# Optimization experiments

Hardware: AMD Instinct MI355X
Metric: run time of the kernel (lower is better)

Reference implementation:

```python
import jax, jax.numpy as jnp
import numpy as np

B, S, H, NH, NL, G, D, A, T = 32, 512, 512, 8, 6, 8, 256, 18, 1024
HD = H // NH


def setup_inputs() -> dict:
    key = jax.random.key(0)
    ks = jax.random.split(key, 32)
    def n(k, shape, s=0.02):
        return jax.random.normal(k, shape, jnp.float32) * s
    return {
        'game_indices': jax.random.randint(ks[0], (B,), 0, G),
        'states': jax.random.normal(ks[1], (B, S, D), jnp.float32),
        'actions': jax.random.randint(ks[2], (B, S), 0, A),
        'returns_to_go': jax.random.normal(ks[3], (B, S), jnp.float32),
        'timesteps': jax.random.randint(ks[4], (B, S), 0, T),
        'attention_mask': jnp.ones((B, S), jnp.int32),
        'game_emb': n(ks[5], (G, H)),
        'obs_W': n(ks[6], (G, D, H)),
        'obs_b': n(ks[7], (G, H)),
        'obs_ln_g': jnp.ones((G, H), jnp.float32),
        'obs_ln_b': jnp.zeros((G, H), jnp.float32),
        'act_emb': n(ks[8], (G, A, H)),
        'ret_W': n(ks[9], (H,)),
        'ret_b': n(ks[10], (H,)),
        'time_emb': n(ks[11], (T, H)),
        'Wqkv': n(ks[12], (NL, 3 * H, H)),
        'bqkv': n(ks[13], (NL, 3 * H)),
        'Wo': n(ks[14], (NL, H, H)),
        'bo': n(ks[15], (NL, H)),
        'ln1_g': jnp.ones((NL, H), jnp.float32),
        'ln1_b': jnp.zeros((NL, H), jnp.float32),
        'W1': n(ks[16], (NL, 4 * H, H)),
        'b1': n(ks[17], (NL, 4 * H)),
        'W2': n(ks[18], (NL, H, 4 * H)),
        'b2': n(ks[19], (NL, H)),
        'ln2_g': jnp.ones((NL, H), jnp.float32),
        'ln2_b': jnp.zeros((NL, H), jnp.float32),
        'sh_W': n(ks[20], (G, H, D)),
        'sh_b': n(ks[21], (G, D)),
        'ah_W': n(ks[22], (G, H, A)),
        'ah_b': n(ks[23], (G, A)),
        'rh_W': n(ks[24], (H, 1)),
        'rh_b': n(ks[25], (1,)),
    }


def _ln(x, g, b, eps=1e-5):
    m = jnp.mean(x, -1, keepdims=True)
    v = jnp.mean((x - m) ** 2, -1, keepdims=True)
    return (x - m) / jnp.sqrt(v + eps) * g + b


def reference(game_indices, states, actions, returns_to_go, timesteps, attention_mask,
              game_emb, obs_W, obs_b, obs_ln_g, obs_ln_b, act_emb, ret_W, ret_b, time_emb,
              Wqkv, bqkv, Wo, bo, ln1_g, ln1_b, W1, b1, W2, b2, ln2_g, ln2_b,
              sh_W, sh_b, ah_W, ah_b, rh_W, rh_b):
    gi = game_indices
    g_emb = game_emb[gi][:, None, :]  # [B,1,H]
    # per-game routed observation embedding: Linear -> LayerNorm -> ReLU (grouped GEMM by game)
    se = jnp.einsum('bsd,bdh->bsh', states, obs_W[gi]) + obs_b[gi][:, None, :]
    se = jax.nn.relu(_ln(se, obs_ln_g[gi][:, None, :], obs_ln_b[gi][:, None, :]))
    # per-game routed action embedding table lookup
    ae = act_emb[gi[:, None], actions]  # [B,S,H]
    re = returns_to_go[..., None] * ret_W + ret_b  # Linear(1,H)
    te = time_emb[timesteps]
    x = se + ae + re + te + g_emb
    # key padding mask (src_key_padding_mask: True where attention_mask==0)
    bias = jnp.where((attention_mask == 0)[:, None, None, :], -1e9, 0.0)  # [B,1,1,S]
    scale = 1.0 / jnp.sqrt(jnp.asarray(HD, jnp.float32))
    for l in range(NL):  # post-norm TransformerEncoderLayer, relu, dropout=0 (eval)
        qkv = jnp.einsum('bsh,oh->bso', x, Wqkv[l]) + bqkv[l]
        q, k, v = jnp.split(qkv, 3, axis=-1)
        q = q.reshape(B, S, NH, HD).transpose(0, 2, 1, 3)
        k = k.reshape(B, S, NH, HD).transpose(0, 2, 1, 3)
        v = v.reshape(B, S, NH, HD).transpose(0, 2, 1, 3)
        scores = jnp.einsum('bhqd,bhkd->bhqk', q, k) * scale + bias
        attn = jnp.einsum('bhqk,bhkd->bhqd', jax.nn.softmax(scores, -1), v)
        attn = attn.transpose(0, 2, 1, 3).reshape(B, S, H)
        attn = jnp.einsum('bsh,oh->bso', attn, Wo[l]) + bo[l]
        x = _ln(x + attn, ln1_g[l], ln1_b[l])
        ff = jax.nn.relu(jnp.einsum('bsh,fh->bsf', x, W1[l]) + b1[l])
        ff = jnp.einsum('bsf,hf->bsh', ff, W2[l]) + b2[l]
        x = _ln(x + ff, ln2_g[l], ln2_b[l])
    # per-game routed prediction heads
    state_preds = jnp.einsum('bsh,bho->bso', x, sh_W[gi]) + sh_b[gi][:, None, :]
    action_preds = jnp.einsum('bsh,bho->bso', x, ah_W[gi]) + ah_b[gi][:, None, :]
    return_preds = x @ rh_W + rh_b
    return (state_preds, action_preds, return_preds)
```

## Files before the change

kernel.cpp:

```cpp
#include <hip/hip_runtime.h>

typedef __bf16 bf16x4 __attribute__((ext_vector_type(4)));
typedef __bf16 bf16x8 __attribute__((ext_vector_type(8)));
typedef float f32x4 __attribute__((ext_vector_type(4)));
typedef int int4v __attribute__((ext_vector_type(4)));

#define C1SM  0.18033688011112042592f

typedef const __attribute__((address_space(1))) void gvoid_t;
typedef __attribute__((address_space(3))) void lvoid_t;


__global__ void cvt_f32_bf16(const float* __restrict__ src, __bf16* __restrict__ dst, int n4)
{
    int i = blockIdx.x * blockDim.x + threadIdx.x;
    if (i >= n4) return;
    f32x4 v = *reinterpret_cast<const f32x4*>(src + (size_t)i * 4);
    bf16x4 o;
    #pragma unroll
    for (int k = 0; k < 4; ++k) o[k] = (__bf16)v[k];
    *reinterpret_cast<bf16x4*>(dst + (size_t)i * 4) = o;
}

__global__ void transpose_cvt(const float* __restrict__ src, __bf16* __restrict__ dst, int R, int C)
{
    int m = blockIdx.y;
    int n = R * C;
    int i = blockIdx.x * 256 + threadIdx.x;
    if (i >= n) return;
    int c = i / R, r = i - c * R;
    dst[(size_t)m * n + i] = (__bf16)src[(size_t)m * n + (size_t)r * C + c];
}

__global__ void transpose_f32(const float* __restrict__ src, float* __restrict__ dst, int R, int C)
{
    int m = blockIdx.y;
    int n = R * C;
    int i = blockIdx.x * 256 + threadIdx.x;
    if (i >= n) return;
    int c = i / R, r = i - c * R;
    dst[(size_t)m * n + i] = src[(size_t)m * n + (size_t)r * C + c];
}

__global__ __launch_bounds__(256, 4)
void gemm_bt(const __bf16* __restrict__ A, size_t strideA,
             const __bf16* __restrict__ B, size_t strideB,
             const float* __restrict__ bias, int strideBias,
             float* Cf, __bf16* Cb, size_t strideC,
             const int* __restrict__ gidx,
             int K, int ldc, int relu, __bf16* __restrict__ vt)
{
    __shared__ __align__(16) char smem[32768];
    __bf16* lCb = (__bf16*)smem;
    float*  lCf = (float*)smem;

    const int z = blockIdx.z;
    const int g = gidx ? gidx[z] : 0;
    const __bf16* Ab = A + (size_t)z * strideA;
    const __bf16* Bb = B + (size_t)g * strideB;

    const int nx = gridDim.x;
    const int nwg = nx * gridDim.y;
    int orig = blockIdx.y * nx + blockIdx.x;
    int wg = ((nwg & 7) == 0) ? ((orig & 7) * (nwg >> 3) + (orig >> 3)) : orig;
    const int bm = (wg / nx) * 128, bn = (wg % nx) * 128;

    const int t = threadIdx.x;
    const int w = t >> 6, lane = t & 63;
    const int wr = (w >> 1) * 64, wc = (w & 1) * 64;
    const int l16 = lane & 15, lk = lane >> 4;

    const int srow = lane >> 2;
    const int schunk = (lane & 3) ^ (srow & 3);
    const int ca = (lk ^ (l16 & 3)) * 8;

    f32x4 acc[4][4] = {};

    auto stage = [&](int buf, int kt) {
        __bf16* la = (__bf16*)(smem + buf * 16384);
        __bf16* lb = la + 4096;
        #pragma unroll
        for (int jj = 0; jj < 2; ++jj) {
            const __bf16* ga = Ab + (size_t)(bm + w * 32 + jj * 16 + srow) * K + kt + schunk * 8;
            __builtin_amdgcn_global_load_lds((gvoid_t*)ga, (lvoid_t*)&la[(w * 32 + jj * 16) * 32], 16, 0, 0);
            const __bf16* gb = Bb + (size_t)(bn + w * 32 + jj * 16 + srow) * K + kt + schunk * 8;
            __builtin_amdgcn_global_load_lds((gvoid_t*)gb, (lvoid_t*)&lb[(w * 32 + jj * 16) * 32], 16, 0, 0);
        }
    };

    stage(0, 0);
    __syncthreads();
    int cur = 0;
    for (int kt = 0; kt < K; kt += 32) {
        if (kt + 32 < K) stage(cur ^ 1, kt + 32);
        __bf16* la = (__bf16*)(smem + cur * 16384);
        __bf16* lb = la + 4096;
        bf16x8 af[4], bfr[4];
        #pragma unroll
        for (int i = 0; i < 4; ++i) {
            af[i]  = *reinterpret_cast<const bf16x8*>(&la[(wr + i * 16 + l16) * 32 + ca]);
            bfr[i] = *reinterpret_cast<const bf16x8*>(&lb[(wc + i * 16 + l16) * 32 + ca]);
        }
        #pragma unroll
        for (int mi = 0; mi < 4; ++mi)
            #pragma unroll
            for (int ni = 0; ni < 4; ++ni)
                acc[mi][ni] = __builtin_amdgcn_mfma_f32_16x16x32_bf16(af[mi], bfr[ni], acc[mi][ni], 0, 0, 0);
        __syncthreads();
        cur ^= 1;
    }

    const float* biasb = bias ? bias + (size_t)g * strideBias : nullptr;

    if (vt && bn >= 1024) {
        const int bb = bm >> 9;
        const int s0 = (bm & 511) + wr + lk * 4;
        #pragma unroll
        for (int ni = 0; ni < 4; ++ni) {
            int c = bn + wc + ni * 16 + l16;
            float bv = biasb ? biasb[c] : 0.f;
            int hh = (c - 1024) >> 6, d = c & 63;
            __bf16* vrow = vt + ((size_t)(bb * 8 + hh) * 64 + d) * 512;
            #pragma unroll
            for (int mi = 0; mi < 4; ++mi) {
                bf16x4 o;
                #pragma unroll
                for (int j = 0; j < 4; ++j) o[j] = (__bf16)(acc[mi][ni][j] + bv);
                *reinterpret_cast<bf16x4*>(vrow + s0 + mi * 16) = o;
            }
        }
        return;
    }

    if (Cb) {
        #pragma unroll
        for (int ni = 0; ni < 4; ++ni) {
            int col = wc + ni * 16 + l16;
            float bv = biasb ? biasb[bn + col] : 0.f;
            #pragma unroll
            for (int mi = 0; mi < 4; ++mi)
                #pragma unroll
                for (int j = 0; j < 4; ++j) {
                    float v = acc[mi][ni][j] + bv;
                    if (relu) v = fmaxf(v, 0.f);
                    lCb[(wr + mi * 16 + lk * 4 + j) * 128 + col] = (__bf16)v;
                }
        }
        __syncthreads();
        #pragma unroll
        for (int it = 0; it < 8; ++it) {
            int off = it * 2048 + t * 8;
            int rl = off >> 7, col = off & 127;
            *reinterpret_cast<int4v*>(Cb + (size_t)z * strideC + (size_t)(bm + rl) * ldc + bn + col) =
                *reinterpret_cast<const int4v*>(&lCb[off]);
        }
    } else {
        #pragma unroll
        for (int p = 0; p < 2; ++p) {
            if (p) __syncthreads();
            if (wr == p * 64) {
                #pragma unroll
                for (int ni = 0; ni < 4; ++ni) {
                    int col = wc + ni * 16 + l16;
                    float bv = biasb ? biasb[bn + col] : 0.f;
                    #pragma unroll
                    for (int mi = 0; mi < 4; ++mi)
                        #pragma unroll
                        for (int j = 0; j < 4; ++j) {
                            float v = acc[mi][ni][j] + bv;
                            if (relu) v = fmaxf(v, 0.f);
                            lCf[(mi * 16 + lk * 4 + j) * 128 + col] = v;
                        }
                }
            }
            __syncthreads();
            #pragma unroll
            for (int it = 0; it < 8; ++it) {
                int off = it * 1024 + t * 4;
                int rl = off >> 7, col = off & 127;
                *reinterpret_cast<f32x4*>(Cf + (size_t)z * strideC + (size_t)(bm + p * 64 + rl) * ldc + bn + col) =
                    *reinterpret_cast<const f32x4*>(&lCf[off]);
            }
        }
    }
}

__global__ __launch_bounds__(256, 4)
void attn_fwd(const __bf16* __restrict__ qkv, const __bf16* __restrict__ vt,
              const int* __restrict__ mask, __bf16* __restrict__ out)
{
    __shared__ __bf16 lK[128 * 64];
    __shared__ __bf16 lP[4][16 * 32];
    __shared__ float lM2[128];

    const int bh = blockIdx.x;
    const int b = bh >> 3, h = bh & 7;
    const int q0 = blockIdx.y * 64;
    const int t = threadIdx.x, w = t >> 6, lane = t & 63;
    const int l16 = lane & 15, lk = lane >> 4;

    const __bf16* qbase = qkv + (size_t)b * 512 * 1536 + h * 64;
    const __bf16* kbase = qbase + 512;
    const __bf16* vtb = vt + (size_t)(b * 8 + h) * 64 * 512;

    bf16x8 qfr[2];
    {
        int row = q0 + w * 16 + l16;
        #pragma unroll
        for (int kc = 0; kc < 2; ++kc)
            qfr[kc] = *reinterpret_cast<const bf16x8*>(qbase + (size_t)row * 1536 + (kc * 4 + lk) * 8);
    }

    float m_run = -1e30f, l_run = 0.f;
    f32x4 oacc[4] = {};
    const int xsw = ((l16 >> 1) & 3) << 1;

    for (int kt = 0; kt < 512; kt += 128) {
        __syncthreads();
        #pragma unroll
        for (int r = 0; r < 4; ++r) {
            int c = t + r * 256;
            int row = c >> 3, ch = c & 7;
            *reinterpret_cast<int4v*>(&lK[row * 64 + ((ch ^ (row & 7)) * 8)]) =
                *reinterpret_cast<const int4v*>(kbase + (size_t)(kt + row) * 1536 + ch * 8);
        }
        if (t < 128) lM2[t] = (mask[b * 512 + kt + t] == 0) ? -2e9f : 0.f;
        __syncthreads();

        f32x4 sacc[8] = {};
        #pragma unroll
        for (int ni = 0; ni < 8; ++ni) {
            int krow = ni * 16 + l16;
            #pragma unroll
            for (int kc = 0; kc < 2; ++kc) {
                bf16x8 kf = *reinterpret_cast<const bf16x8*>(&lK[krow * 64 + (((kc * 4 + lk) ^ (krow & 7)) * 8)]);
                sacc[ni] = __builtin_amdgcn_mfma_f32_16x16x32_bf16(kf, qfr[kc], sacc[ni], 0, 0, 0);
            }
        }

        float mx = -3e38f;
        #pragma unroll
        for (int ni = 0; ni < 8; ++ni) {
            f32x4 mkv = *reinterpret_cast<const f32x4*>(&lM2[ni * 16 + lk * 4]);
            #pragma unroll
            for (int j = 0; j < 4; ++j) {
                float sv = fmaf(sacc[ni][j], C1SM, mkv[j]);
                sacc[ni][j] = sv;
                mx = fmaxf(mx, sv);
            }
        }
        mx = fmaxf(mx, __shfl_xor(mx, 16));
        mx = fmaxf(mx, __shfl_xor(mx, 32));
        bool need = mx > m_run + 11.54f;
        if (__any((int)need)) {
            float mn = fmaxf(m_run, mx);
            float alpha = exp2f(m_run - mn);
            m_run = mn;
            l_run *= alpha;
            #pragma unroll
            for (int j = 0; j < 4; ++j) {
                float aj = __shfl(alpha, lk * 4 + j);
                #pragma unroll
                for (int dn = 0; dn < 4; ++dn) oacc[dn][j] *= aj;
            }
        }
        float ps = 0.f;
        #pragma unroll
        for (int ni = 0; ni < 8; ++ni)
            #pragma unroll
            for (int j = 0; j < 4; ++j) {
                float p = exp2f(sacc[ni][j] - m_run);
                sacc[ni][j] = p;
                ps += p;
            }
        l_run += ps;

        __bf16* lp = &lP[w][0];
        #pragma unroll
        for (int kc = 0; kc < 4; ++kc) {
            #pragma unroll
            for (int n2 = 0; n2 < 2; ++n2) {
                bf16x4 o;
                #pragma unroll
                for (int j = 0; j < 4; ++j) o[j] = (__bf16)sacc[kc * 2 + n2][j];
                *reinterpret_cast<bf16x4*>(&lp[l16 * 32 + ((n2 * 4 + lk) ^ xsw) * 4]) = o;
            }
            bf16x8 pf = *reinterpret_cast<const bf16x8*>(&lp[l16 * 32 + (lk ^ (xsw >> 1)) * 8]);
            #pragma unroll
            for (int dn = 0; dn < 4; ++dn) {
                bf16x8 vf = *reinterpret_cast<const bf16x8*>(vtb + (size_t)(dn * 16 + l16) * 512 + kt + kc * 32 + lk * 8);
                oacc[dn] = __builtin_amdgcn_mfma_f32_16x16x32_bf16(pf, vf, oacc[dn], 0, 0, 0);
            }
        }
    }

    float s = l_run;
    s += __shfl_xor(s, 16);
    s += __shfl_xor(s, 32);
    float linv = 1.f / s;
    #pragma unroll
    for (int j = 0; j < 4; ++j) {
        float lj = __shfl(linv, lk * 4 + j);
        #pragma unroll
        for (int dn = 0; dn < 4; ++dn) {
            int row = q0 + w * 16 + lk * 4 + j;
            int col = h * 64 + dn * 16 + l16;
            out[(size_t)(b * 512 + row) * 512 + col] = (__bf16)(oacc[dn][j] * lj);
        }
    }
}


__device__ __forceinline__ float wsum64(float v)
{
    #pragma unroll
    for (int d = 32; d >= 1; d >>= 1) v += __shfl_xor(v, d);
    return v;
}

__global__ __launch_bounds__(256)
void ln_fuse(const float* resid, const __bf16* __restrict__ proj,
             const float* __restrict__ gamma, const float* __restrict__ beta,
             float* xfo, __bf16* __restrict__ xbo)
{
    int tok = blockIdx.x * 4 + (threadIdx.x >> 6);
    int lane = threadIdx.x & 63;
    size_t base = (size_t)tok * 512 + lane * 8;
    float y[8];
    {
        f32x4 a0 = *reinterpret_cast<const f32x4*>(resid + base);
        f32x4 a1 = *reinterpret_cast<const f32x4*>(resid + base + 4);
        bf16x8 pv = *reinterpret_cast<const bf16x8*>(proj + base);
        #pragma unroll
        for (int i = 0; i < 4; ++i) { y[i] = a0[i] + (float)pv[i]; y[4 + i] = a1[i] + (float)pv[4 + i]; }
    }
    float s = 0.f;
    #pragma unroll
    for (int i = 0; i < 8; ++i) s += y[i];
    float mean = wsum64(s) * (1.f / 512.f);
    float v = 0.f;
    #pragma unroll
    for (int i = 0; i < 8; ++i) { float d = y[i] - mean; v += d * d; }
    float rstd = rsqrtf(wsum64(v) * (1.f / 512.f) + 1e-5f);
    int hh = lane * 8;
    f32x4 g0 = *reinterpret_cast<const f32x4*>(gamma + hh);
    f32x4 g1 = *reinterpret_cast<const f32x4*>(gamma + hh + 4);
    f32x4 b0 = *reinterpret_cast<const f32x4*>(beta + hh);
    f32x4 b1 = *reinterpret_cast<const f32x4*>(beta + hh + 4);
    f32x4 o0, o1;
    bf16x8 ob;
    #pragma unroll
    for (int i = 0; i < 4; ++i) {
        float t0 = (y[i] - mean) * rstd * g0[i] + b0[i];
        float t1 = (y[4 + i] - mean) * rstd * g1[i] + b1[i];
        o0[i] = t0; o1[i] = t1;
        ob[i] = (__bf16)t0; ob[4 + i] = (__bf16)t1;
    }
    *reinterpret_cast<f32x4*>(xfo + base) = o0;
    *reinterpret_cast<f32x4*>(xfo + base + 4) = o1;
    *reinterpret_cast<bf16x8*>(xbo + base) = ob;
}

__global__ __launch_bounds__(256)
void embed_fin(const __bf16* __restrict__ seraw, const int* __restrict__ gi,
               const int* __restrict__ actions, const float* __restrict__ rtg,
               const int* __restrict__ ts,
               const float* __restrict__ olg, const float* __restrict__ olb,
               const float* __restrict__ act_emb, const float* __restrict__ retW,
               const float* __restrict__ retb, const float* __restrict__ time_emb,
               const float* __restrict__ game_emb,
               float* __restrict__ xfo, __bf16* __restrict__ xbo)
{
    int tok = blockIdx.x * 4 + (threadIdx.x >> 6);
    int lane = threadIdx.x & 63;
    int b = tok >> 9;
    int g = gi[b];
    int a = actions[tok];
    int tt = ts[tok];
    float rv = rtg[tok];
    size_t base = (size_t)tok * 512 + lane * 8;
    int hh = lane * 8;

    float y[8];
    {
        bf16x8 a0 = *reinterpret_cast<const bf16x8*>(seraw + base);
        #pragma unroll
        for (int i = 0; i < 8; ++i) y[i] = (float)a0[i];
    }
    float s = 0.f;
    #pragma unroll
    for (int i = 0; i < 8; ++i) s += y[i];
    float mean = wsum64(s) * (1.f / 512.f);
    float v = 0.f;
    #pragma unroll
    for (int i = 0; i < 8; ++i) { float d = y[i] - mean; v += d * d; }
    float rstd = rsqrtf(wsum64(v) * (1.f / 512.f) + 1e-5f);

    const float* gp = olg + (size_t)g * 512 + hh;
    const float* bp = olb + (size_t)g * 512 + hh;
    const float* ap = act_emb + ((size_t)g * 18 + a) * 512 + hh;
    const float* tp = time_emb + (size_t)tt * 512 + hh;
    const float* ep = game_emb + (size_t)g * 512 + hh;
    const float* rwp = retW + hh;
    const float* rbp = retb + hh;

    f32x4 o0, o1;
    bf16x8 ob;
    #pragma unroll
    for (int half = 0; half < 2; ++half) {
        f32x4 gv = *reinterpret_cast<const f32x4*>(gp + half * 4);
        f32x4 bv = *reinterpret_cast<const f32x4*>(bp + half * 4);
        f32x4 av = *reinterpret_cast<const f32x4*>(ap + half * 4);
        f32x4 tv = *reinterpret_cast<const f32x4*>(tp + half * 4);
        f32x4 ev = *reinterpret_cast<const f32x4*>(ep + half * 4);
        f32x4 rw = *reinterpret_cast<const f32x4*>(rwp + half * 4);
        f32x4 rb = *reinterpret_cast<const f32x4*>(rbp + half * 4);
        #pragma unroll
        for (int i = 0; i < 4; ++i) {
            float n = (y[half * 4 + i] - mean) * rstd * gv[i] + bv[i];
            n = fmaxf(n, 0.f);
            float o = n + av[i] + rv * rw[i] + rb[i] + tv[i] + ev[i];
            if (half == 0) o0[i] = o; else o1[i] = o;
            ob[half * 4 + i] = (__bf16)o;
        }
    }
    *reinterpret_cast<f32x4*>(xfo + base) = o0;
    *reinterpret_cast<f32x4*>(xfo + base + 4) = o1;
    *reinterpret_cast<bf16x8*>(xbo + base) = ob;
}

__global__ __launch_bounds__(256)
void head_ar(const float* __restrict__ xf, const int* __restrict__ gi,
             const float* __restrict__ ahWt, const float* __restrict__ ah_b,
             const float* __restrict__ rhW, const float* __restrict__ rhb,
             float* __restrict__ outA, float* __restrict__ outR)
{
    int tok = blockIdx.x * 4 + (threadIdx.x >> 6);
    int lane = threadIdx.x & 63;
    int b = tok >> 9;
    int g = gi[b];
    size_t base = (size_t)tok * 512 + lane * 8;
    float x[8];
    {
        f32x4 a0 = *reinterpret_cast<const f32x4*>(xf + base);
        f32x4 a1 = *reinterpret_cast<const f32x4*>(xf + base + 4);
        #pragma unroll
        for (int i = 0; i < 4; ++i) { x[i] = a0[i]; x[4 + i] = a1[i]; }
    }
    #pragma unroll 1
    for (int a = 0; a < 18; ++a) {
        const float* wp = ahWt + ((size_t)g * 18 + a) * 512 + lane * 8;
        f32x4 w0 = *reinterpret_cast<const f32x4*>(wp);
        f32x4 w1 = *reinterpret_cast<const f32x4*>(wp + 4);
        float p = 0.f;
        #pragma unroll
        for (int i = 0; i < 4; ++i) { p += x[i] * w0[i]; p += x[4 + i] * w1[i]; }
        p = wsum64(p);
        if (lane == 0) outA[(size_t)tok * 18 + a] = p + ah_b[g * 18 + a];
    }
    {
        const float* wp = rhW + lane * 8;
        f32x4 w0 = *reinterpret_cast<const f32x4*>(wp);
        f32x4 w1 = *reinterpret_cast<const f32x4*>(wp + 4);
        float p = 0.f;
        #pragma unroll
        for (int i = 0; i < 4; ++i) { p += x[i] * w0[i]; p += x[4 + i] * w1[i]; }
        p = wsum64(p);
        if (lane == 0) outR[tok] = p + rhb[0];
    }
}


extern "C" void kernel_launch(void* const* d_in, const int* in_sizes, int n_in,
                              void* d_out, int out_size, void* d_ws, size_t ws_size,
                              hipStream_t stream)
{
    (void)in_sizes; (void)n_in; (void)out_size; (void)ws_size;

    const int*   gi       = (const int*)d_in[0];
    const float* states   = (const float*)d_in[1];
    const int*   actions  = (const int*)d_in[2];
    const float* rtg      = (const float*)d_in[3];
    const int*   ts       = (const int*)d_in[4];
    const int*   amask    = (const int*)d_in[5];
    const float* game_emb = (const float*)d_in[6];
    const float* obs_W    = (const float*)d_in[7];
    const float* obs_b    = (const float*)d_in[8];
    const float* obs_ln_g = (const float*)d_in[9];
    const float* obs_ln_b = (const float*)d_in[10];
    const float* act_emb  = (const float*)d_in[11];
    const float* ret_W    = (const float*)d_in[12];
    const float* ret_b    = (const float*)d_in[13];
    const float* time_emb = (const float*)d_in[14];
    const float* Wqkv     = (const float*)d_in[15];
    const float* bqkv     = (const float*)d_in[16];
    const float* Wo       = (const float*)d_in[17];
    const float* bo       = (const float*)d_in[18];
    const float* ln1_g    = (const float*)d_in[19];
    const float* ln1_b    = (const float*)d_in[20];
    const float* W1       = (const float*)d_in[21];
    const float* b1       = (const float*)d_in[22];
    const float* W2       = (const float*)d_in[23];
    const float* b2       = (const float*)d_in[24];
    const float* ln2_g    = (const float*)d_in[25];
    const float* ln2_b    = (const float*)d_in[26];
    const float* sh_W     = (const float*)d_in[27];
    const float* sh_b     = (const float*)d_in[28];
    const float* ah_W     = (const float*)d_in[29];
    const float* ah_b     = (const float*)d_in[30];
    const float* rh_W     = (const float*)d_in[31];
    const float* rh_b     = (const float*)d_in[32];

    char* wsb = (char*)d_ws;
    float*  xf      = (float*)(wsb + 0);
    __bf16* xb      = (__bf16*)(wsb + 33554432);
    __bf16* tmp     = (__bf16*)(wsb + 50331648);
    __bf16* vT      = (__bf16*)(wsb + 67108864);
    __bf16* qkvB    = (__bf16*)(wsb + 83886080);
    __bf16* ff1B    = qkvB;
    __bf16* statesB = qkvB;
    __bf16* obswB   = (__bf16*)(wsb + 83886080 + 8388608);
    __bf16* attnB   = (__bf16*)(wsb + 150994944);
    __bf16* wqkvB   = (__bf16*)(wsb + 167772160);
    __bf16* woB     = (__bf16*)(wsb + 177209344);
    __bf16* w1B     = (__bf16*)(wsb + 180355072);
    __bf16* w2B     = (__bf16*)(wsb + 192937984);
    __bf16* shwB    = (__bf16*)(wsb + 205520896);
    float*  ahwT    = (float*)(wsb + 207618048);

    cvt_f32_bf16<<<4608, 256, 0, stream>>>(Wqkv, wqkvB, 1179648);
    cvt_f32_bf16<<<1536, 256, 0, stream>>>(Wo, woB, 393216);
    cvt_f32_bf16<<<6144, 256, 0, stream>>>(W1, w1B, 1572864);
    cvt_f32_bf16<<<6144, 256, 0, stream>>>(W2, w2B, 1572864);
    cvt_f32_bf16<<<4096, 256, 0, stream>>>(states, statesB, 1048576);
    transpose_cvt<<<dim3(512, 8), 256, 0, stream>>>(obs_W, obswB, 256, 512);
    transpose_cvt<<<dim3(512, 8), 256, 0, stream>>>(sh_W, shwB, 512, 256);
    transpose_f32<<<dim3(36, 8), 256, 0, stream>>>(ah_W, ahwT, 512, 18);

    gemm_bt<<<dim3(4, 4, 32), 256, 0, stream>>>(
        statesB, (size_t)512 * 256, obswB, (size_t)512 * 256, obs_b, 512,
        nullptr, tmp, (size_t)512 * 512, gi, 256, 512, 0, nullptr);
    embed_fin<<<4096, 256, 0, stream>>>(tmp, gi, actions, rtg, ts,
        obs_ln_g, obs_ln_b, act_emb, ret_W, ret_b, time_emb, game_emb, xf, xb);

    for (int l = 0; l < 6; ++l) {
        gemm_bt<<<dim3(12, 128, 1), 256, 0, stream>>>(
            xb, 0, wqkvB + (size_t)l * 1536 * 512, 0, bqkv + l * 1536, 0,
            nullptr, qkvB, 0, nullptr, 512, 1536, 0, vT);
        attn_fwd<<<dim3(256, 8, 1), 256, 0, stream>>>(qkvB, vT, amask, attnB);
        gemm_bt<<<dim3(4, 128, 1), 256, 0, stream>>>(
            attnB, 0, woB + (size_t)l * 512 * 512, 0, bo + l * 512, 0,
            nullptr, tmp, 0, nullptr, 512, 512, 0, nullptr);
        ln_fuse<<<4096, 256, 0, stream>>>(xf, tmp, ln1_g + l * 512, ln1_b + l * 512, xf, xb);
        gemm_bt<<<dim3(16, 128, 1), 256, 0, stream>>>(
            xb, 0, w1B + (size_t)l * 2048 * 512, 0, b1 + l * 2048, 0,
            nullptr, ff1B, 0, nullptr, 512, 2048, 1, nullptr);
        gemm_bt<<<dim3(4, 128, 1), 256, 0, stream>>>(
            ff1B, 0, w2B + (size_t)l * 512 * 2048, 0, b2 + l * 512, 0,
            nullptr, tmp, 0, nullptr, 2048, 512, 0, nullptr);
        ln_fuse<<<4096, 256, 0, stream>>>(xf, tmp, ln2_g + l * 512, ln2_b + l * 512, xf, xb);
    }

    gemm_bt<<<dim3(2, 4, 32), 256, 0, stream>>>(
        xb, (size_t)512 * 512, shwB, (size_t)256 * 512, sh_b, 256,
        (float*)d_out, nullptr, (size_t)512 * 256, gi, 512, 256, 0, nullptr);
    head_ar<<<4096, 256, 0, stream>>>(xf, gi, ahwT, ah_b, rh_W, rh_b,
        (float*)d_out + 4194304, (float*)d_out + 4489216);
}
```

Before: 1.670 ms.

## Double-buffer K tiles in attention via async global-to-LDS loads

The attention kernel now stages K in 64-row tiles into two LDS buffers with global_load_lds, prefetching the next tile while the current one is computed. This replaces the 128-row single buffer that needed a sync before and after each load. The whole mask row is preloaded once, the max and sum reductions are split into independent partial accumulators, and the launch-bounds occupancy hint rises from 4 to 6. This gives more, smaller iterations, each with its own barrier, and may raise register pressure under the higher occupancy target.

```diff
diff --git a/kernel.cpp b/kernel.cpp
--- a/kernel.cpp
+++ b/kernel.cpp
@@ -185,13 +185,13 @@
     }
 }
 
-__global__ __launch_bounds__(256, 4)
+__global__ __launch_bounds__(256, 6)
 void attn_fwd(const __bf16* __restrict__ qkv, const __bf16* __restrict__ vt,
               const int* __restrict__ mask, __bf16* __restrict__ out)
 {
-    __shared__ __bf16 lK[128 * 64];
+    __shared__ __bf16 lK[2][64 * 64];
     __shared__ __bf16 lP[4][16 * 32];
-    __shared__ float lM2[128];
+    __shared__ float lM2[512];
 
     const int bh = blockIdx.x;
     const int b = bh >> 3, h = bh & 7;
@@ -211,44 +211,59 @@
             qfr[kc] = *reinterpret_cast<const bf16x8*>(qbase + (size_t)row * 1536 + (kc * 4 + lk) * 8);
     }
 
+    {
+        int i0 = t * 2;
+        lM2[i0]     = (mask[b * 512 + i0] == 0)     ? -2e9f : 0.f;
+        lM2[i0 + 1] = (mask[b * 512 + i0 + 1] == 0) ? -2e9f : 0.f;
+    }
+
+    auto stageK = [&](int buf, int kt) {
+        #pragma unroll
+        for (int r = 0; r < 2; ++r) {
+            int c = r * 256 + w * 64 + lane;
+            int row = c >> 3, ch = c & 7;
+            const __bf16* ga = kbase + (size_t)(kt + row) * 1536 + ((ch ^ (row & 7)) * 8);
+            __builtin_amdgcn_global_load_lds((gvoid_t*)ga,
+                (lvoid_t*)(&lK[buf][0] + (r * 256 + w * 64) * 8), 16, 0, 0);
+        }
+    };
+
     float m_run = -1e30f, l_run = 0.f;
     f32x4 oacc[4] = {};
     const int xsw = ((l16 >> 1) & 3) << 1;
 
-    for (int kt = 0; kt < 512; kt += 128) {
-        __syncthreads();
-        #pragma unroll
-        for (int r = 0; r < 4; ++r) {
-            int c = t + r * 256;
-            int row = c >> 3, ch = c & 7;
-            *reinterpret_cast<int4v*>(&lK[row * 64 + ((ch ^ (row & 7)) * 8)]) =
-                *reinterpret_cast<const int4v*>(kbase + (size_t)(kt + row) * 1536 + ch * 8);
-        }
-        if (t < 128) lM2[t] = (mask[b * 512 + kt + t] == 0) ? -2e9f : 0.f;
-        __syncthreads();
-
-        f32x4 sacc[8] = {};
-        #pragma unroll
-        for (int ni = 0; ni < 8; ++ni) {
+    stageK(0, 0);
+    __syncthreads();
+
+    int cur = 0;
+    for (int kt = 0; kt < 512; kt += 64) {
+        if (kt + 64 < 512) stageK(cur ^ 1, kt + 64);
+        const __bf16* lKc = &lK[cur][0];
+
+        f32x4 sacc[4] = {};
+        #pragma unroll
+        for (int ni = 0; ni < 4; ++ni) {
             int krow = ni * 16 + l16;
             #pragma unroll
             for (int kc = 0; kc < 2; ++kc) {
-                bf16x8 kf = *reinterpret_cast<const bf16x8*>(&lK[krow * 64 + (((kc * 4 + lk) ^ (krow & 7)) * 8)]);
+                bf16x8 kf = *reinterpret_cast<const bf16x8*>(&lKc[krow * 64 + (((kc * 4 + lk) ^ (krow & 7)) * 8)]);
                 sacc[ni] = __builtin_amdgcn_mfma_f32_16x16x32_bf16(kf, qfr[kc], sacc[ni], 0, 0, 0);
             }
         }
 
-        float mx = -3e38f;
-        #pragma unroll
-        for (int ni = 0; ni < 8; ++ni) {
-            f32x4 mkv = *reinterpret_cast<const f32x4*>(&lM2[ni * 16 + lk * 4]);
+        f32x4 mx4 = {-3e38f, -3e38f, -3e38f, -3e38f};
+        #pragma unroll
+        for (int ni = 0; ni < 4; ++ni) {
+            f32x4 mkv = *reinterpret_cast<const f32x4*>(&lM2[kt + ni * 16 + lk * 4]);
+            f32x4 sv;
             #pragma unroll
             for (int j = 0; j < 4; ++j) {
-                float sv = fmaf(sacc[ni][j], C1SM, mkv[j]);
-                sacc[ni][j] = sv;
-                mx = fmaxf(mx, sv);
-            }
-        }
+                sv[j] = fmaf(sacc[ni][j], C1SM, mkv[j]);
+                mx4[j] = fmaxf(mx4[j], sv[j]);
+            }
+            sacc[ni] = sv;
+        }
+        float mx = fmaxf(fmaxf(mx4[0], mx4[1]), fmaxf(mx4[2], mx4[3]));
         mx = fmaxf(mx, __shfl_xor(mx, 16));
         mx = fmaxf(mx, __shfl_xor(mx, 32));
         bool need = mx > m_run + 11.54f;
@@ -264,20 +279,20 @@
                 for (int dn = 0; dn < 4; ++dn) oacc[dn][j] *= aj;
             }
         }
-        float ps = 0.f;
-        #pragma unroll
-        for (int ni = 0; ni < 8; ++ni)
+        f32x4 ps4 = {0.f, 0.f, 0.f, 0.f};
+        #pragma unroll
+        for (int ni = 0; ni < 4; ++ni)
             #pragma unroll
             for (int j = 0; j < 4; ++j) {
                 float p = exp2f(sacc[ni][j] - m_run);
                 sacc[ni][j] = p;
-                ps += p;
-            }
-        l_run += ps;
+                ps4[j] += p;
+            }
+        l_run += (ps4[0] + ps4[1]) + (ps4[2] + ps4[3]);
 
         __bf16* lp = &lP[w][0];
         #pragma unroll
-        for (int kc = 0; kc < 4; ++kc) {
+        for (int kc = 0; kc < 2; ++kc) {
             #pragma unroll
             for (int n2 = 0; n2 < 2; ++n2) {
                 bf16x4 o;
@@ -292,6 +307,8 @@
                 oacc[dn] = __builtin_amdgcn_mfma_f32_16x16x32_bf16(pf, vf, oacc[dn], 0, 0, 0);
             }
         }
+        __syncthreads();
+        cur ^= 1;
     }
 
     float s = l_run;
```

New measurement: 1.666 ms. No clear change (-0.2%).
